# Kernel tuning notes

Measured on AMD Instinct MI355X. Metric: run time of the kernel, lower is better.

## Reference

```python
import jax, jax.numpy as jnp
import numpy as np

M0, M1, M2 = 128, 64, 32            # multiplicities of 0e, 1o, 2e
NUM_IRREPS = M0 + M1 + M2           # 224
NODE_DIM = 128
SPH_DIM = M0 + 3 * M1 + 5 * M2      # 480
HIDDEN = 2 * NODE_DIM + NUM_IRREPS  # 480
N = 100000
EPS = 1e-5
SQ3 = float(np.sqrt(3.0))
SQ5 = float(np.sqrt(5.0))


def _split(x):
    s0 = x[:, :M0]                                   # [N,128]   l=0
    s1 = x[:, M0:M0 + 3 * M1].reshape(-1, M1, 3)     # [N,64,3]  l=1
    s2 = x[:, M0 + 3 * M1:].reshape(-1, M2, 5)       # [N,32,5]  l=2
    return s0, s1, s2


def _merge(s0, s1, s2):
    n = s0.shape[0]
    return jnp.concatenate([s0, s1.reshape(n, -1), s2.reshape(n, -1)], axis=-1)


def _o3_linear(s0, s1, s2, w0, w1, w2, b0):
    # e3nn o3.Linear: one path per l, element path-normalization 1/sqrt(mul_in); bias only on 0e
    y0 = s0 @ w0 / np.float32(np.sqrt(M0)) + b0
    y1 = jnp.einsum('nik,io->nok', s1, w1) / np.float32(np.sqrt(M1))
    y2 = jnp.einsum('nik,io->nok', s2, w2) / np.float32(np.sqrt(M2))
    return y0, y1, y2


def _o3_layernorm(s0, s1, s2, w, b):
    # equivariant layer norm: mean-center scalars only; RMS over (mul, components) per irrep type
    f0 = s0 - jnp.mean(s0, axis=1, keepdims=True)
    n0 = jnp.mean(f0 * f0, axis=1, keepdims=True)
    f0 = f0 * jax.lax.rsqrt(n0 + EPS) * w[:M0] + b
    n1 = jnp.mean(s1 * s1, axis=(1, 2))[:, None, None]
    f1 = s1 * jax.lax.rsqrt(n1 + EPS) * w[M0:M0 + M1][None, :, None]
    n2 = jnp.mean(s2 * s2, axis=(1, 2))[:, None, None]
    f2 = s2 * jax.lax.rsqrt(n2 + EPS) * w[M0 + M1:][None, :, None]
    return f0, f1, f2


def setup_inputs() -> dict:
    key = jax.random.key(0)
    ks = jax.random.split(key, 16)
    g = lambda k, shape: jax.random.normal(k, shape, jnp.float32)
    return {
        'x_scalar': g(ks[0], (N, NODE_DIM)),
        'x_spherical': g(ks[1], (N, SPH_DIM)),
        'ln_g': jnp.ones((NODE_DIM,), jnp.float32),
        'ln_b': jnp.zeros((NODE_DIM,), jnp.float32),
        'o3n_w': jnp.ones((NUM_IRREPS,), jnp.float32),
        'o3n_b': jnp.zeros((M0,), jnp.float32),
        'U_w0': g(ks[2], (M0, M0)), 'U_w1': g(ks[3], (M1, M1)), 'U_w2': g(ks[4], (M2, M2)),
        'U_b0': jnp.zeros((M0,), jnp.float32),
        'V_w0': g(ks[5], (M0, M0)), 'V_w1': g(ks[6], (M1, M1)), 'V_w2': g(ks[7], (M2, M2)),
        'V_b0': jnp.zeros((M0,), jnp.float32),
        'dot_w': g(ks[8], (NUM_IRREPS, NODE_DIM)) / np.float32(np.sqrt(NUM_IRREPS)),
        'mlp_w1': g(ks[9], (NODE_DIM + NUM_IRREPS, NODE_DIM)) / np.float32(np.sqrt(NODE_DIM + NUM_IRREPS)),
        'mlp_b1': jnp.zeros((NODE_DIM,), jnp.float32),
        'mlp_w2': g(ks[10], (NODE_DIM, HIDDEN)) / np.float32(np.sqrt(NODE_DIM)),
        'mlp_b2': jnp.zeros((HIDDEN,), jnp.float32),
    }


def reference(x_scalar, x_spherical, ln_g, ln_b, o3n_w, o3n_b,
              U_w0, U_w1, U_w2, U_b0, V_w0, V_w1, V_w2, V_b0,
              dot_w, mlp_w1, mlp_b1, mlp_w2, mlp_b2):
    # scalar layer norm
    mu = jnp.mean(x_scalar, axis=-1, keepdims=True)
    var = jnp.var(x_scalar, axis=-1, keepdims=True)
    scalar_in = (x_scalar - mu) * jax.lax.rsqrt(var + EPS) * ln_g + ln_b
    # equivariant layer norm on spherical features
    s0, s1, s2 = _split(x_spherical)
    s0, s1, s2 = _o3_layernorm(s0, s1, s2, o3n_w, o3n_b)
    U0, U1, U2 = _o3_linear(s0, s1, s2, U_w0, U_w1, U_w2, U_b0)
    V0, V1, V2 = _o3_linear(s0, s1, s2, V_w0, V_w1, V_w2, V_b0)
    # o3.Norm: per-irrep L2 norm -> [N, 224]
    inv = jnp.concatenate([jnp.abs(V0),
                           jnp.sqrt(jnp.sum(V1 * V1, axis=-1)),
                           jnp.sqrt(jnp.sum(V2 * V2, axis=-1))], axis=-1)
    mlp_in = jnp.concatenate([scalar_in, inv], axis=-1)          # [N, 352]
    h = jax.nn.silu(mlp_in @ mlp_w1 + mlp_b1)
    mlp_out = h @ mlp_w2 + mlp_b2                                # [N, 480]
    a_vv = mlp_out[:, :NUM_IRREPS]
    a_sv = mlp_out[:, NUM_IRREPS:NUM_IRREPS + NODE_DIM]
    a_ss = mlp_out[:, NUM_IRREPS + NODE_DIM:]
    # ElementwiseTensorProduct with 224x0e: per-irrep scalar gating (net factor 1)
    d0 = U0 * a_vv[:, :M0]
    d1 = U1 * a_vv[:, M0:M0 + M1, None]
    d2 = U2 * a_vv[:, M0 + M1:, None]
    # EquivariantDot (component-normalized uuu TP to 0e): dot / sqrt(2l+1)
    dot = jnp.concatenate([U0 * V0,
                           jnp.sum(U1 * V1, axis=-1) / SQ3,
                           jnp.sum(U2 * V2, axis=-1) / SQ5], axis=-1)
    inner = dot @ dot_w                                           # [N, 128]
    d_scalar = a_sv * inner + a_ss
    return x_scalar + d_scalar, x_spherical + _merge(d0, d1, d2)
```

## Files before the change

kernel.cpp:

```cpp
#include <hip/hip_runtime.h>
#include <stdint.h>

typedef unsigned short u16;
typedef __attribute__((ext_vector_type(2))) unsigned short u16x2;
typedef __attribute__((ext_vector_type(4))) unsigned short u16x4;
typedef __attribute__((ext_vector_type(8))) short s16x8;
typedef __attribute__((ext_vector_type(2))) float f32x2;
typedef __attribute__((ext_vector_type(4))) float f32x4;

#define NROWS 100000
#define RPB   32
#define NBLK  (NROWS / RPB)
#define NTHR  512

#define PF   488
#define PS   360
#define PH   136
#define PD   232
#define PAB  484
#define PIF  132
#define FIN_RG  (16 * PF)
#define SCB_RG  (16 * PS)
#define HB_RG   (16 * PH)
#define DOT_RG  (16 * PD)
#define AOUT_RG (16 * PAB)
#define INN_RG  (16 * PIF)

#define OFF_FIN   0
#define OFF_AOUT  0
#define OFF_SCB   31232
#define OFF_INNER 31232
#define OFF_DOTB  54272
#define OFF_HB    69120
#define OFF_BCOM  77824
#define ARENA_SZ  79552

#define B_UW0 0
#define B_UW1 16384
#define B_UW2 20480
#define B_VW0 21504
#define B_VW1 37888
#define B_VW2 41984
#define B_DW  43008
#define B_W1  71680
#define B_W2  116736
#define PACK_TOT 178176

__device__ inline float bf2f(u16 u) {
    union { uint32_t i; float f; } v; v.i = (uint32_t)u << 16; return v.f;
}
__device__ inline u16 f2bf(float f) {
    union { float f; uint32_t i; } v; v.f = f;
    return (u16)((v.i + 0x7fffu + ((v.i >> 16) & 1u)) >> 16);
}
__device__ inline float wsum32(float v) {
    #pragma unroll
    for (int m = 16; m >= 1; m >>= 1) v += __shfl_xor(v, m);
    return v;
}
__device__ inline bool detect_f32(const void* xs) {
    const u16 v = ((const u16*)xs)[threadIdx.x & 63];
    const float f = bf2f(v);
    return __any(!(fabsf(f) < 1e10f)) != 0;
}
__device__ inline float ldin(const void* p, size_t i, bool f32) {
    return f32 ? ((const float*)p)[i] : bf2f(((const u16*)p)[i]);
}
__device__ inline void stout(void* p, size_t i, float v, bool f32) {
    if (f32) ((float*)p)[i] = v; else ((u16*)p)[i] = f2bf(v);
}

struct Ptrs {
    const void *xs, *xp, *lng, *lnb, *o3w, *o3b;
    const void *Uw0, *Uw1, *Uw2, *Ub0, *Vw0, *Vw1, *Vw2, *Vb0;
    const void *dw, *w1, *b1, *w2, *b2;
    const u16 *ws;
    void *out;
};

template<int KS, bool PACKED>
__device__ inline void load_b(const void* W, int D, int tile, int lane, bool wf32, s16x8* bfr)
{
    #pragma unroll
    for (int ks = 0; ks < KS; ++ks) {
        if (PACKED) {
            bfr[ks] = *(const s16x8*)((const u16*)W + (((size_t)tile * KS + ks) * 64 + (size_t)lane) * 8);
        } else {
            union { u16 u[8]; s16x8 v; } bb;
            const int k0 = ks * 32 + ((lane >> 4) << 3), o = tile * 16 + (lane & 15);
            #pragma unroll
            for (int j = 0; j < 8; ++j) {
                const size_t idx = (size_t)(k0 + j) * D + o;
                bb.u[j] = wf32 ? f2bf(((const float*)W)[idx]) : ((const u16*)W)[idx];
            }
            bfr[ks] = bb.v;
        }
    }
}

template<int KS>
__device__ inline f32x4 acc_ab(const u16* A, int pitchA, int lane, const s16x8* bfr)
{
    f32x4 acc = {0.f, 0.f, 0.f, 0.f};
    const u16* arow = A + (lane & 15) * pitchA + (lane >> 4) * 8;
    #pragma unroll
    for (int ks = 0; ks < KS; ++ks) {
        s16x8 a = *(const s16x8*)(arow + ks * 32);
        acc = __builtin_amdgcn_mfma_f32_16x16x32_bf16(a, bfr[ks], acc, 0, 0, 0);
    }
    return acc;
}

template<int KS, bool PACKED>
__device__ inline void mm_silu(const u16* A, int pitchA, const void* W, int D,
                               int tile, int lane, const u16* bias, u16* outH, bool wf32)
{
    s16x8 bfr[KS];
    load_b<KS, PACKED>(W, D, tile, lane, wf32, bfr);
    f32x4 acc = acc_ab<KS>(A, pitchA, lane, bfr);
    const int r = lane & 15, g = lane >> 4;
    const int o = tile * 16 + r;
    const float bv = bf2f(bias[o]);
    #pragma unroll
    for (int q = 0; q < 4; ++q) {
        float x = acc[q] + bv;
        outH[(g * 4 + q) * PH + o] = f2bf(x / (1.f + expf(-x)));
    }
}

__global__ void pack_weights(Ptrs P, u16* ws)
{
    const bool wf32 = detect_f32(P.xs);
    const int gid = blockIdx.x * 256 + threadIdx.x;
    if (gid >= PACK_TOT) return;
    const int  base[10] = {B_UW0, B_UW1, B_UW2, B_VW0, B_VW1, B_VW2, B_DW, B_W1, B_W2, PACK_TOT};
    const int  Kd[9]    = {128, 64, 32, 128, 64, 32, 224, 352, 128};
    const void* srcs[9] = {P.Uw0, P.Uw1, P.Uw2, P.Vw0, P.Vw1, P.Vw2, P.dw, P.w1, P.w2};
    const int  Dstride[9] = {128, 64, 32, 128, 64, 32, 128, 128, 480};
    int m = 0;
    for (int i = 1; i < 9; ++i) if (gid >= base[i]) m = i;
    const int e = gid - base[m];
    const int j = e & 7, lane = (e >> 3) & 63, tk = e >> 9;
    const int Ks = Kd[m] >> 5;
    const int ks = tk % Ks, tile = tk / Ks;
    const int k = ks * 32 + ((lane >> 4) << 3) + j;
    const int o = tile * 16 + (lane & 15);
    const size_t idx = (size_t)k * Dstride[m] + o;
    ws[gid] = wf32 ? f2bf(((const float*)srcs[m])[idx]) : ((const u16*)srcs[m])[idx];
}

template<int DT>
__device__ inline void stage1_core(const Ptrs& P, u16* fin0, u16* scb0, int tid, int row0)
{
    const int hw = tid >> 5, l32 = tid & 31;
    #pragma unroll
    for (int rg = 0; rg < 2; ++rg) {
        const int rr = hw + rg * 16;
        const size_t row = (size_t)(row0 + rr);
        u16* finr = fin0 + rg * FIN_RG + hw * PF;
        u16* scbr = scb0 + rg * SCB_RG + hw * PS;
        const u16*   xsb = (const u16*)P.xs + row * 128;
        const float* xsf = (const float*)P.xs + row * 128;
        const u16*   xpb = (const u16*)P.xp + row * 480;
        const float* xpf = (const float*)P.xp + row * 480;
        {
            float v[4];
            if (DT) { f32x4 u = *(const f32x4*)(xsf + l32 * 4); v[0]=u[0];v[1]=u[1];v[2]=u[2];v[3]=u[3]; }
            else    { u16x4 u = *(const u16x4*)(xsb + l32 * 4);
                      v[0]=bf2f(u[0]);v[1]=bf2f(u[1]);v[2]=bf2f(u[2]);v[3]=bf2f(u[3]); }
            float s  = v[0] + v[1] + v[2] + v[3];
            float s2 = v[0]*v[0] + v[1]*v[1] + v[2]*v[2] + v[3]*v[3];
            s = wsum32(s); s2 = wsum32(s2);
            const float mu = s * (1.f / 128.f);
            const float rs = 1.f / sqrtf(s2 * (1.f / 128.f) - mu * mu + 1e-5f);
            const int c = l32 * 4;
            #pragma unroll
            for (int j2 = 0; j2 < 4; ++j2)
                scbr[c + j2] =
                    f2bf((v[j2] - mu) * rs * ldin(P.lng, c + j2, DT) + ldin(P.lnb, c + j2, DT));
        }
        {
            float v[4];
            if (DT) { f32x4 u = *(const f32x4*)(xpf + l32 * 4); v[0]=u[0];v[1]=u[1];v[2]=u[2];v[3]=u[3]; }
            else    { u16x4 u = *(const u16x4*)(xpb + l32 * 4);
                      v[0]=bf2f(u[0]);v[1]=bf2f(u[1]);v[2]=bf2f(u[2]);v[3]=bf2f(u[3]); }
            float s  = v[0] + v[1] + v[2] + v[3];
            float s2 = v[0]*v[0] + v[1]*v[1] + v[2]*v[2] + v[3]*v[3];
            s = wsum32(s); s2 = wsum32(s2);
            const float mu = s * (1.f / 128.f);
            const float rs = 1.f / sqrtf(s2 * (1.f / 128.f) - mu * mu + 1e-5f);
            const int c = l32 * 4;
            #pragma unroll
            for (int j2 = 0; j2 < 4; ++j2)
                finr[c + j2] =
                    f2bf((v[j2] - mu) * rs * ldin(P.o3w, c + j2, DT) + ldin(P.o3b, c + j2, DT));
        }
        {
            const int cb = l32 * 6;
            float w[6];
            if (DT) {
                f32x2 a0 = *(const f32x2*)(xpf + 128 + cb);
                f32x2 a1 = *(const f32x2*)(xpf + 128 + cb + 2);
                f32x2 a2 = *(const f32x2*)(xpf + 128 + cb + 4);
                w[0]=a0[0]; w[1]=a0[1]; w[2]=a1[0]; w[3]=a1[1]; w[4]=a2[0]; w[5]=a2[1];
            } else {
                u16x2 a0 = *(const u16x2*)(xpb + 128 + cb);
                u16x2 a1 = *(const u16x2*)(xpb + 128 + cb + 2);
                u16x2 a2 = *(const u16x2*)(xpb + 128 + cb + 4);
                w[0]=bf2f(a0[0]); w[1]=bf2f(a0[1]); w[2]=bf2f(a1[0]);
                w[3]=bf2f(a1[1]); w[4]=bf2f(a2[0]); w[5]=bf2f(a2[1]);
            }
            float ss = 0.f;
            #pragma unroll
            for (int j2 = 0; j2 < 6; ++j2) ss += w[j2] * w[j2];
            ss = wsum32(ss);
            const float rs = 1.f / sqrtf(ss * (1.f / 192.f) + 1e-5f);
            #pragma unroll
            for (int j2 = 0; j2 < 6; ++j2) {
                const int c = cb + j2, i = c / 3, k = c - 3 * i;
                finr[128 + k * 64 + i] = f2bf(w[j2] * rs * ldin(P.o3w, 128 + i, DT));
            }
        }
        {
            const int cb = l32 * 5;
            float w[5];
            #pragma unroll
            for (int j2 = 0; j2 < 5; ++j2)
                w[j2] = DT ? xpf[320 + cb + j2] : bf2f(xpb[320 + cb + j2]);
            float ss = 0.f;
            #pragma unroll
            for (int j2 = 0; j2 < 5; ++j2) ss += w[j2] * w[j2];
            ss = wsum32(ss);
            const float rs = 1.f / sqrtf(ss * (1.f / 160.f) + 1e-5f);
            #pragma unroll
            for (int j2 = 0; j2 < 5; ++j2) {
                const int c = cb + j2, i = c / 5, k = c - 5 * i;
                finr[320 + k * 32 + i] = f2bf(w[j2] * rs * ldin(P.o3w, 192 + i, DT));
            }
        }
    }
}

template<bool PACKED>
__global__ __launch_bounds__(NTHR, 4) void xpainn_main(Ptrs P)
{
    __shared__ __align__(16) unsigned char arena[ARENA_SZ];
    u16*   fin    = (u16*)(arena + OFF_FIN);
    u16*   aoutB  = (u16*)(arena + OFF_AOUT);
    u16*   scb    = (u16*)(arena + OFF_SCB);
    float* innerF = (float*)(arena + OFF_INNER);
    u16*   dotb   = (u16*)(arena + OFF_DOTB);
    u16*   hb     = (u16*)(arena + OFF_HB);
    u16*   bcom   = (u16*)(arena + OFF_BCOM);

    const int tid = threadIdx.x;
    const int lane = tid & 63, wave = tid >> 6;
    const int r = lane & 15, g = lane >> 4;
    const int row0 = blockIdx.x * RPB;
    const bool isf32 = detect_f32(P.xs);

    for (int i = tid; i < 864; i += NTHR) {
        const void* src; int off;
        if (i < 128)      { src = P.Ub0; off = i; }
        else if (i < 256) { src = P.Vb0; off = i - 128; }
        else if (i < 384) { src = P.b1;  off = i - 256; }
        else              { src = P.b2;  off = i - 384; }
        bcom[i] = f2bf(ldin(src, off, isf32));
    }
    if (isf32) stage1_core<1>(P, fin, scb, tid, row0);
    else       stage1_core<0>(P, fin, scb, tid, row0);
    __syncthreads();

    float u0r[2][4];
    float uxr[2][5][4];
    {
        s16x8 bU[4], bV[4];
        load_b<4, PACKED>(PACKED ? (const void*)(P.ws + B_UW0) : P.Uw0, 128, wave, lane, isf32, bU);
        load_b<4, PACKED>(PACKED ? (const void*)(P.ws + B_VW0) : P.Vw0, 128, wave, lane, isf32, bV);
        const int o = wave * 16 + r;
        const float bu = bf2f(bcom[o]), bv = bf2f(bcom[128 + o]);
        #pragma unroll
        for (int rg = 0; rg < 2; ++rg) {
            f32x4 au = acc_ab<4>(fin + rg * FIN_RG, PF, lane, bU);
            f32x4 av = acc_ab<4>(fin + rg * FIN_RG, PF, lane, bV);
            u16* scbR = scb + rg * SCB_RG;
            u16* dotR = dotb + rg * DOT_RG;
            #pragma unroll
            for (int q = 0; q < 4; ++q) {
                const float U = au[q] * 0.08838834764831845f + bu;
                const float V = av[q] * 0.08838834764831845f + bv;
                u0r[rg][q] = U;
                const int lrow = g * 4 + q;
                scbR[lrow * PS + 128 + o] = f2bf(fabsf(V));
                dotR[lrow * PD + o]       = f2bf(U * V);
            }
        }
    }
    if (wave < 4) {
        const int tt = wave, o = tt * 16 + r;
        float sv[2][4] = {{0.f,0.f,0.f,0.f},{0.f,0.f,0.f,0.f}};
        float suv[2][4] = {{0.f,0.f,0.f,0.f},{0.f,0.f,0.f,0.f}};
        #pragma unroll
        for (int ch = 0; ch < 3; ++ch) {
            s16x8 bU[2], bV[2];
            load_b<2, PACKED>(PACKED ? (const void*)(P.ws + B_UW1) : P.Uw1, 64, tt, lane, isf32, bU);
            load_b<2, PACKED>(PACKED ? (const void*)(P.ws + B_VW1) : P.Vw1, 64, tt, lane, isf32, bV);
            #pragma unroll
            for (int rg = 0; rg < 2; ++rg) {
                f32x4 au = acc_ab<2>(fin + rg * FIN_RG + 128 + 64 * ch, PF, lane, bU);
                f32x4 av = acc_ab<2>(fin + rg * FIN_RG + 128 + 64 * ch, PF, lane, bV);
                #pragma unroll
                for (int q = 0; q < 4; ++q) {
                    const float U = au[q] * 0.125f, V = av[q] * 0.125f;
                    uxr[rg][ch][q] = U; sv[rg][q] += V * V; suv[rg][q] += U * V;
                }
            }
        }
        #pragma unroll
        for (int rg = 0; rg < 2; ++rg) {
            #pragma unroll
            for (int q = 0; q < 4; ++q) {
                const int lrow = g * 4 + q;
                (scb + rg * SCB_RG)[lrow * PS + 256 + o]  = f2bf(sqrtf(sv[rg][q]));
                (dotb + rg * DOT_RG)[lrow * PD + 128 + o] = f2bf(suv[rg][q] * 0.5773502691896258f);
            }
        }
    } else if (wave < 6) {
        const int tt = wave - 4, o = tt * 16 + r;
        float sv[2][4] = {{0.f,0.f,0.f,0.f},{0.f,0.f,0.f,0.f}};
        float suv[2][4] = {{0.f,0.f,0.f,0.f},{0.f,0.f,0.f,0.f}};
        #pragma unroll
        for (int ch = 0; ch < 5; ++ch) {
            s16x8 bU[1], bV[1];
            load_b<1, PACKED>(PACKED ? (const void*)(P.ws + B_UW2) : P.Uw2, 32, tt, lane, isf32, bU);
            load_b<1, PACKED>(PACKED ? (const void*)(P.ws + B_VW2) : P.Vw2, 32, tt, lane, isf32, bV);
            #pragma unroll
            for (int rg = 0; rg < 2; ++rg) {
                f32x4 au = acc_ab<1>(fin + rg * FIN_RG + 320 + 32 * ch, PF, lane, bU);
                f32x4 av = acc_ab<1>(fin + rg * FIN_RG + 320 + 32 * ch, PF, lane, bV);
                #pragma unroll
                for (int q = 0; q < 4; ++q) {
                    const float U = au[q] * 0.17677669529663687f, V = av[q] * 0.17677669529663687f;
                    uxr[rg][ch][q] = U; sv[rg][q] += V * V; suv[rg][q] += U * V;
                }
            }
        }
        #pragma unroll
        for (int rg = 0; rg < 2; ++rg) {
            #pragma unroll
            for (int q = 0; q < 4; ++q) {
                const int lrow = g * 4 + q;
                (scb + rg * SCB_RG)[lrow * PS + 320 + o]  = f2bf(sqrtf(sv[rg][q]));
                (dotb + rg * DOT_RG)[lrow * PD + 192 + o] = f2bf(suv[rg][q] * 0.4472135954999579f);
            }
        }
    }
    __syncthreads();

    #pragma unroll
    for (int rg = 0; rg < 2; ++rg)
        mm_silu<11, PACKED>(scb + rg * SCB_RG, PS, PACKED ? (const void*)(P.ws + B_W1) : P.w1,
                            128, wave, lane, bcom + 256, hb + rg * HB_RG, isf32);
    __syncthreads();

    for (int ti = wave; ti < 38; ti += 8) {
        if (ti < 30) {
            s16x8 bfr[4];
            load_b<4, PACKED>(PACKED ? (const void*)(P.ws + B_W2) : P.w2, 480, ti, lane, isf32, bfr);
            const int o = ti * 16 + r;
            const float bv = bf2f(bcom[384 + o]);
            #pragma unroll
            for (int rg = 0; rg < 2; ++rg) {
                f32x4 acc = acc_ab<4>(hb + rg * HB_RG, PH, lane, bfr);
                u16* aoutR = aoutB + rg * AOUT_RG;
                #pragma unroll
                for (int q = 0; q < 4; ++q)
                    aoutR[(g * 4 + q) * PAB + o] = f2bf(acc[q] + bv);
            }
        } else {
            s16x8 bfr[7];
            load_b<7, PACKED>(PACKED ? (const void*)(P.ws + B_DW) : P.dw, 128, ti - 30, lane, isf32, bfr);
            const int o = (ti - 30) * 16 + r;
            #pragma unroll
            for (int rg = 0; rg < 2; ++rg) {
                f32x4 acc = acc_ab<7>(dotb + rg * DOT_RG, PD, lane, bfr);
                float* innR = innerF + rg * INN_RG;
                #pragma unroll
                for (int q = 0; q < 4; ++q)
                    innR[(g * 4 + q) * PIF + o] = acc[q];
            }
        }
    }
    __syncthreads();

    #pragma unroll
    for (int it = 0; it < 2; ++it) {
        const int idx = tid + it * NTHR;
        const int r2 = idx >> 5, c4 = (idx & 31) * 4;
        const u16*  aoutR = aoutB + (r2 >> 4) * AOUT_RG + (r2 & 15) * PAB;
        const float* innR = innerF + (r2 >> 4) * INN_RG + (r2 & 15) * PIF;
        const size_t gb = (size_t)(row0 + r2) * 128 + c4;
        const u16x4 asv = *(const u16x4*)(aoutR + 224 + c4);
        const u16x4 ass = *(const u16x4*)(aoutR + 352 + c4);
        const f32x4 inn = *(const f32x4*)(innR + c4);
        if (isf32) {
            const f32x4 xs = *(const f32x4*)((const float*)P.xs + gb);
            f32x4 o;
            #pragma unroll
            for (int j = 0; j < 4; ++j) o[j] = xs[j] + bf2f(asv[j]) * inn[j] + bf2f(ass[j]);
            *(f32x4*)((float*)P.out + gb) = o;
        } else {
            const u16x4 xs = *(const u16x4*)((const u16*)P.xs + gb);
            u16x4 o;
            #pragma unroll
            for (int j = 0; j < 4; ++j) o[j] = f2bf(bf2f(xs[j]) + bf2f(asv[j]) * inn[j] + bf2f(ass[j]));
            *(u16x4*)((u16*)P.out + gb) = o;
        }
    }
    {
        const size_t ob = (size_t)NROWS * 128;
        #pragma unroll
        for (int rg = 0; rg < 2; ++rg) {
            const u16* aoutR = aoutB + rg * AOUT_RG;
            const int o = wave * 16 + r;
            #pragma unroll
            for (int q = 0; q < 4; ++q) {
                const int lrow = g * 4 + q;
                const size_t gr = (size_t)(row0 + rg * 16 + lrow) * 480;
                const float av = bf2f(aoutR[lrow * PAB + o]);
                stout(P.out, ob + gr + o, ldin(P.xp, gr + o, isf32) + u0r[rg][q] * av, isf32);
            }
            if (wave < 4) {
                const int i = wave * 16 + r;
                #pragma unroll
                for (int q = 0; q < 4; ++q) {
                    const int lrow = g * 4 + q;
                    const size_t gr = (size_t)(row0 + rg * 16 + lrow) * 480;
                    const float av = bf2f(aoutR[lrow * PAB + 128 + i]);
                    #pragma unroll
                    for (int ch = 0; ch < 3; ++ch) {
                        const size_t c = 128 + 3 * i + ch;
                        stout(P.out, ob + gr + c, ldin(P.xp, gr + c, isf32) + uxr[rg][ch][q] * av, isf32);
                    }
                }
            } else if (wave < 6) {
                const int i = (wave - 4) * 16 + r;
                #pragma unroll
                for (int q = 0; q < 4; ++q) {
                    const int lrow = g * 4 + q;
                    const size_t gr = (size_t)(row0 + rg * 16 + lrow) * 480;
                    const float av = bf2f(aoutR[lrow * PAB + 192 + i]);
                    #pragma unroll
                    for (int ch = 0; ch < 5; ++ch) {
                        const size_t c = 320 + 5 * i + ch;
                        stout(P.out, ob + gr + c, ldin(P.xp, gr + c, isf32) + uxr[rg][ch][q] * av, isf32);
                    }
                }
            }
        }
    }
}

extern "C" void kernel_launch(void* const* d_in, const int* in_sizes, int n_in,
                              void* d_out, int out_size, void* d_ws, size_t ws_size,
                              hipStream_t stream)
{
    Ptrs P;
    P.xs  = d_in[0];  P.xp  = d_in[1];
    P.lng = d_in[2];  P.lnb = d_in[3];
    P.o3w = d_in[4];  P.o3b = d_in[5];
    P.Uw0 = d_in[6];  P.Uw1 = d_in[7];
    P.Uw2 = d_in[8];  P.Ub0 = d_in[9];
    P.Vw0 = d_in[10]; P.Vw1 = d_in[11];
    P.Vw2 = d_in[12]; P.Vb0 = d_in[13];
    P.dw  = d_in[14]; P.w1  = d_in[15];
    P.b1  = d_in[16]; P.w2  = d_in[17];
    P.b2  = d_in[18];
    P.ws  = (const u16*)d_ws;
    P.out = d_out;

    const bool packed = (ws_size >= (size_t)PACK_TOT * sizeof(u16));
    if (packed) {
        pack_weights<<<(PACK_TOT + 255) / 256, 256, 0, stream>>>(P, (u16*)d_ws);
        xpainn_main<true><<<NBLK, NTHR, 0, stream>>>(P);
    } else {
        xpainn_main<false><<<NBLK, NTHR, 0, stream>>>(P);
    }
}
```

Before: 235.9 us.

## Specialize for fp32 I/O, use hardware bf16 converts, fuse spherical output into MLP stage

Drops runtime bf16/fp32 detection and assumes fp32 inputs and outputs, removing per-element dtype branches. Replaces the software bf16 rounding with the v_cvt_pk_bf16_f32 instruction and packs pairs of bf16 stores, and vectorizes the l=1/l=2 loads. Restructures the second MLP matmul so each wave keeps its a_vv gate tiles in registers and writes the spherical output right away, skipping the bf16 round trip through LDS for those gates. This loses the bf16 input path and changes gate precision slightly.

Measured after the change: 220.3 us, median of 2. 6.6% less time.

```diff
diff --git a/kernel.cpp b/kernel.cpp
--- a/kernel.cpp
+++ b/kernel.cpp
@@ -2,11 +2,11 @@
 #include <stdint.h>
 
 typedef unsigned short u16;
-typedef __attribute__((ext_vector_type(2))) unsigned short u16x2;
 typedef __attribute__((ext_vector_type(4))) unsigned short u16x4;
 typedef __attribute__((ext_vector_type(8))) short s16x8;
 typedef __attribute__((ext_vector_type(2))) float f32x2;
 typedef __attribute__((ext_vector_type(4))) float f32x4;
+typedef __attribute__((ext_vector_type(4), aligned(4))) float f32x4u;
 
 #define NROWS 100000
 #define RPB   32
@@ -50,36 +50,27 @@
     union { uint32_t i; float f; } v; v.i = (uint32_t)u << 16; return v.f;
 }
 __device__ inline u16 f2bf(float f) {
-    union { float f; uint32_t i; } v; v.f = f;
-    return (u16)((v.i + 0x7fffu + ((v.i >> 16) & 1u)) >> 16);
+    uint32_t d; asm("v_cvt_pk_bf16_f32 %0, %1, %1" : "=v"(d) : "v"(f)); return (u16)d;
+}
+__device__ inline uint32_t cvtpk(float lo, float hi) {
+    uint32_t d; asm("v_cvt_pk_bf16_f32 %0, %1, %2" : "=v"(d) : "v"(lo), "v"(hi)); return d;
 }
 __device__ inline float wsum32(float v) {
     #pragma unroll
     for (int m = 16; m >= 1; m >>= 1) v += __shfl_xor(v, m);
     return v;
 }
-__device__ inline bool detect_f32(const void* xs) {
-    const u16 v = ((const u16*)xs)[threadIdx.x & 63];
-    const float f = bf2f(v);
-    return __any(!(fabsf(f) < 1e10f)) != 0;
-}
-__device__ inline float ldin(const void* p, size_t i, bool f32) {
-    return f32 ? ((const float*)p)[i] : bf2f(((const u16*)p)[i]);
-}
-__device__ inline void stout(void* p, size_t i, float v, bool f32) {
-    if (f32) ((float*)p)[i] = v; else ((u16*)p)[i] = f2bf(v);
-}
 
 struct Ptrs {
-    const void *xs, *xp, *lng, *lnb, *o3w, *o3b;
-    const void *Uw0, *Uw1, *Uw2, *Ub0, *Vw0, *Vw1, *Vw2, *Vb0;
-    const void *dw, *w1, *b1, *w2, *b2;
+    const float *xs, *xp, *lng, *lnb, *o3w, *o3b;
+    const float *Uw0, *Uw1, *Uw2, *Ub0, *Vw0, *Vw1, *Vw2, *Vb0;
+    const float *dw, *w1, *b1, *w2, *b2;
     const u16 *ws;
-    void *out;
+    float *out;
 };
 
 template<int KS, bool PACKED>
-__device__ inline void load_b(const void* W, int D, int tile, int lane, bool wf32, s16x8* bfr)
+__device__ inline void load_b(const void* W, int D, int tile, int lane, s16x8* bfr)
 {
     #pragma unroll
     for (int ks = 0; ks < KS; ++ks) {
@@ -89,10 +80,8 @@
             union { u16 u[8]; s16x8 v; } bb;
             const int k0 = ks * 32 + ((lane >> 4) << 3), o = tile * 16 + (lane & 15);
             #pragma unroll
-            for (int j = 0; j < 8; ++j) {
-                const size_t idx = (size_t)(k0 + j) * D + o;
-                bb.u[j] = wf32 ? f2bf(((const float*)W)[idx]) : ((const u16*)W)[idx];
-            }
+            for (int j = 0; j < 8; ++j)
+                bb.u[j] = f2bf(((const float*)W)[(size_t)(k0 + j) * D + o]);
             bfr[ks] = bb.v;
         }
     }
@@ -111,31 +100,13 @@
     return acc;
 }
 
-template<int KS, bool PACKED>
-__device__ inline void mm_silu(const u16* A, int pitchA, const void* W, int D,
-                               int tile, int lane, const u16* bias, u16* outH, bool wf32)
-{
-    s16x8 bfr[KS];
-    load_b<KS, PACKED>(W, D, tile, lane, wf32, bfr);
-    f32x4 acc = acc_ab<KS>(A, pitchA, lane, bfr);
-    const int r = lane & 15, g = lane >> 4;
-    const int o = tile * 16 + r;
-    const float bv = bf2f(bias[o]);
-    #pragma unroll
-    for (int q = 0; q < 4; ++q) {
-        float x = acc[q] + bv;
-        outH[(g * 4 + q) * PH + o] = f2bf(x / (1.f + expf(-x)));
-    }
-}
-
 __global__ void pack_weights(Ptrs P, u16* ws)
 {
-    const bool wf32 = detect_f32(P.xs);
     const int gid = blockIdx.x * 256 + threadIdx.x;
     if (gid >= PACK_TOT) return;
     const int  base[10] = {B_UW0, B_UW1, B_UW2, B_VW0, B_VW1, B_VW2, B_DW, B_W1, B_W2, PACK_TOT};
     const int  Kd[9]    = {128, 64, 32, 128, 64, 32, 224, 352, 128};
-    const void* srcs[9] = {P.Uw0, P.Uw1, P.Uw2, P.Vw0, P.Vw1, P.Vw2, P.dw, P.w1, P.w2};
+    const float* srcs[9] = {P.Uw0, P.Uw1, P.Uw2, P.Vw0, P.Vw1, P.Vw2, P.dw, P.w1, P.w2};
     const int  Dstride[9] = {128, 64, 32, 128, 64, 32, 128, 128, 480};
     int m = 0;
     for (int i = 1; i < 9; ++i) if (gid >= base[i]) m = i;
@@ -145,11 +116,9 @@
     const int ks = tk % Ks, tile = tk / Ks;
     const int k = ks * 32 + ((lane >> 4) << 3) + j;
     const int o = tile * 16 + (lane & 15);
-    const size_t idx = (size_t)k * Dstride[m] + o;
-    ws[gid] = wf32 ? f2bf(((const float*)srcs[m])[idx]) : ((const u16*)srcs[m])[idx];
-}
-
-template<int DT>
+    ws[gid] = f2bf(srcs[m][(size_t)k * Dstride[m] + o]);
+}
+
 __device__ inline void stage1_core(const Ptrs& P, u16* fin0, u16* scb0, int tid, int row0)
 {
     const int hw = tid >> 5, l32 = tid & 31;
@@ -159,57 +128,43 @@
         const size_t row = (size_t)(row0 + rr);
         u16* finr = fin0 + rg * FIN_RG + hw * PF;
         u16* scbr = scb0 + rg * SCB_RG + hw * PS;
-        const u16*   xsb = (const u16*)P.xs + row * 128;
-        const float* xsf = (const float*)P.xs + row * 128;
-        const u16*   xpb = (const u16*)P.xp + row * 480;
-        const float* xpf = (const float*)P.xp + row * 480;
-        {
-            float v[4];
-            if (DT) { f32x4 u = *(const f32x4*)(xsf + l32 * 4); v[0]=u[0];v[1]=u[1];v[2]=u[2];v[3]=u[3]; }
-            else    { u16x4 u = *(const u16x4*)(xsb + l32 * 4);
-                      v[0]=bf2f(u[0]);v[1]=bf2f(u[1]);v[2]=bf2f(u[2]);v[3]=bf2f(u[3]); }
-            float s  = v[0] + v[1] + v[2] + v[3];
-            float s2 = v[0]*v[0] + v[1]*v[1] + v[2]*v[2] + v[3]*v[3];
+        const float* xsf = P.xs + row * 128;
+        const float* xpf = P.xp + row * 480;
+        {
+            f32x4 u = *(const f32x4*)(xsf + l32 * 4);
+            float s  = u[0] + u[1] + u[2] + u[3];
+            float s2 = u[0]*u[0] + u[1]*u[1] + u[2]*u[2] + u[3]*u[3];
             s = wsum32(s); s2 = wsum32(s2);
             const float mu = s * (1.f / 128.f);
             const float rs = 1.f / sqrtf(s2 * (1.f / 128.f) - mu * mu + 1e-5f);
             const int c = l32 * 4;
+            float t[4];
             #pragma unroll
             for (int j2 = 0; j2 < 4; ++j2)
-                scbr[c + j2] =
-                    f2bf((v[j2] - mu) * rs * ldin(P.lng, c + j2, DT) + ldin(P.lnb, c + j2, DT));
-        }
-        {
-            float v[4];
-            if (DT) { f32x4 u = *(const f32x4*)(xpf + l32 * 4); v[0]=u[0];v[1]=u[1];v[2]=u[2];v[3]=u[3]; }
-            else    { u16x4 u = *(const u16x4*)(xpb + l32 * 4);
-                      v[0]=bf2f(u[0]);v[1]=bf2f(u[1]);v[2]=bf2f(u[2]);v[3]=bf2f(u[3]); }
-            float s  = v[0] + v[1] + v[2] + v[3];
-            float s2 = v[0]*v[0] + v[1]*v[1] + v[2]*v[2] + v[3]*v[3];
+                t[j2] = (u[j2] - mu) * rs * P.lng[c + j2] + P.lnb[c + j2];
+            *(uint32_t*)(scbr + c)     = cvtpk(t[0], t[1]);
+            *(uint32_t*)(scbr + c + 2) = cvtpk(t[2], t[3]);
+        }
+        {
+            f32x4 u = *(const f32x4*)(xpf + l32 * 4);
+            float s  = u[0] + u[1] + u[2] + u[3];
+            float s2 = u[0]*u[0] + u[1]*u[1] + u[2]*u[2] + u[3]*u[3];
             s = wsum32(s); s2 = wsum32(s2);
             const float mu = s * (1.f / 128.f);
             const float rs = 1.f / sqrtf(s2 * (1.f / 128.f) - mu * mu + 1e-5f);
             const int c = l32 * 4;
+            float t[4];
             #pragma unroll
             for (int j2 = 0; j2 < 4; ++j2)
-                finr[c + j2] =
-                    f2bf((v[j2] - mu) * rs * ldin(P.o3w, c + j2, DT) + ldin(P.o3b, c + j2, DT));
+                t[j2] = (u[j2] - mu) * rs * P.o3w[c + j2] + P.o3b[c + j2];
+            *(uint32_t*)(finr + c)     = cvtpk(t[0], t[1]);
+            *(uint32_t*)(finr + c + 2) = cvtpk(t[2], t[3]);
         }
         {
             const int cb = l32 * 6;
-            float w[6];
-            if (DT) {
-                f32x2 a0 = *(const f32x2*)(xpf + 128 + cb);
-                f32x2 a1 = *(const f32x2*)(xpf + 128 + cb + 2);
-                f32x2 a2 = *(const f32x2*)(xpf + 128 + cb + 4);
-                w[0]=a0[0]; w[1]=a0[1]; w[2]=a1[0]; w[3]=a1[1]; w[4]=a2[0]; w[5]=a2[1];
-            } else {
-                u16x2 a0 = *(const u16x2*)(xpb + 128 + cb);
-                u16x2 a1 = *(const u16x2*)(xpb + 128 + cb + 2);
-                u16x2 a2 = *(const u16x2*)(xpb + 128 + cb + 4);
-                w[0]=bf2f(a0[0]); w[1]=bf2f(a0[1]); w[2]=bf2f(a1[0]);
-                w[3]=bf2f(a1[1]); w[4]=bf2f(a2[0]); w[5]=bf2f(a2[1]);
-            }
+            f32x4u a = *(const f32x4u*)(xpf + 128 + cb);
+            f32x2  b = *(const f32x2*)(xpf + 128 + cb + 4);
+            float w[6] = {a[0], a[1], a[2], a[3], b[0], b[1]};
             float ss = 0.f;
             #pragma unroll
             for (int j2 = 0; j2 < 6; ++j2) ss += w[j2] * w[j2];
@@ -218,15 +173,13 @@
             #pragma unroll
             for (int j2 = 0; j2 < 6; ++j2) {
                 const int c = cb + j2, i = c / 3, k = c - 3 * i;
-                finr[128 + k * 64 + i] = f2bf(w[j2] * rs * ldin(P.o3w, 128 + i, DT));
+                finr[128 + k * 64 + i] = f2bf(w[j2] * rs * P.o3w[128 + i]);
             }
         }
         {
             const int cb = l32 * 5;
-            float w[5];
-            #pragma unroll
-            for (int j2 = 0; j2 < 5; ++j2)
-                w[j2] = DT ? xpf[320 + cb + j2] : bf2f(xpb[320 + cb + j2]);
+            f32x4u a = *(const f32x4u*)(xpf + 320 + cb);
+            float w[5] = {a[0], a[1], a[2], a[3], xpf[320 + cb + 4]};
             float ss = 0.f;
             #pragma unroll
             for (int j2 = 0; j2 < 5; ++j2) ss += w[j2] * w[j2];
@@ -235,7 +188,7 @@
             #pragma unroll
             for (int j2 = 0; j2 < 5; ++j2) {
                 const int c = cb + j2, i = c / 5, k = c - 5 * i;
-                finr[320 + k * 32 + i] = f2bf(w[j2] * rs * ldin(P.o3w, 192 + i, DT));
+                finr[320 + k * 32 + i] = f2bf(w[j2] * rs * P.o3w[192 + i]);
             }
         }
     }
@@ -257,26 +210,24 @@
     const int lane = tid & 63, wave = tid >> 6;
     const int r = lane & 15, g = lane >> 4;
     const int row0 = blockIdx.x * RPB;
-    const bool isf32 = detect_f32(P.xs);
 
     for (int i = tid; i < 864; i += NTHR) {
-        const void* src; int off;
+        const float* src; int off;
         if (i < 128)      { src = P.Ub0; off = i; }
         else if (i < 256) { src = P.Vb0; off = i - 128; }
         else if (i < 384) { src = P.b1;  off = i - 256; }
         else              { src = P.b2;  off = i - 384; }
-        bcom[i] = f2bf(ldin(src, off, isf32));
-    }
-    if (isf32) stage1_core<1>(P, fin, scb, tid, row0);
-    else       stage1_core<0>(P, fin, scb, tid, row0);
+        bcom[i] = f2bf(src[off]);
+    }
+    stage1_core(P, fin, scb, tid, row0);
     __syncthreads();
 
     float u0r[2][4];
     float uxr[2][5][4];
     {
         s16x8 bU[4], bV[4];
-        load_b<4, PACKED>(PACKED ? (const void*)(P.ws + B_UW0) : P.Uw0, 128, wave, lane, isf32, bU);
-        load_b<4, PACKED>(PACKED ? (const void*)(P.ws + B_VW0) : P.Vw0, 128, wave, lane, isf32, bV);
+        load_b<4, PACKED>(PACKED ? (const void*)(P.ws + B_UW0) : (const void*)P.Uw0, 128, wave, lane, bU);
+        load_b<4, PACKED>(PACKED ? (const void*)(P.ws + B_VW0) : (const void*)P.Vw0, 128, wave, lane, bV);
         const int o = wave * 16 + r;
         const float bu = bf2f(bcom[o]), bv = bf2f(bcom[128 + o]);
         #pragma unroll
@@ -303,8 +254,8 @@
         #pragma unroll
         for (int ch = 0; ch < 3; ++ch) {
             s16x8 bU[2], bV[2];
-            load_b<2, PACKED>(PACKED ? (const void*)(P.ws + B_UW1) : P.Uw1, 64, tt, lane, isf32, bU);
-            load_b<2, PACKED>(PACKED ? (const void*)(P.ws + B_VW1) : P.Vw1, 64, tt, lane, isf32, bV);
+            load_b<2, PACKED>(PACKED ? (const void*)(P.ws + B_UW1) : (const void*)P.Uw1, 64, tt, lane, bU);
+            load_b<2, PACKED>(PACKED ? (const void*)(P.ws + B_VW1) : (const void*)P.Vw1, 64, tt, lane, bV);
             #pragma unroll
             for (int rg = 0; rg < 2; ++rg) {
                 f32x4 au = acc_ab<2>(fin + rg * FIN_RG + 128 + 64 * ch, PF, lane, bU);
@@ -332,8 +283,8 @@
         #pragma unroll
         for (int ch = 0; ch < 5; ++ch) {
             s16x8 bU[1], bV[1];
-            load_b<1, PACKED>(PACKED ? (const void*)(P.ws + B_UW2) : P.Uw2, 32, tt, lane, isf32, bU);
-            load_b<1, PACKED>(PACKED ? (const void*)(P.ws + B_VW2) : P.Vw2, 32, tt, lane, isf32, bV);
+            load_b<1, PACKED>(PACKED ? (const void*)(P.ws + B_UW2) : (const void*)P.Uw2, 32, tt, lane, bU);
+            load_b<1, PACKED>(PACKED ? (const void*)(P.ws + B_VW2) : (const void*)P.Vw2, 32, tt, lane, bV);
             #pragma unroll
             for (int rg = 0; rg < 2; ++rg) {
                 f32x4 au = acc_ab<1>(fin + rg * FIN_RG + 320 + 32 * ch, PF, lane, bU);
@@ -358,36 +309,115 @@
     __syncthreads();
 
     #pragma unroll
-    for (int rg = 0; rg < 2; ++rg)
-        mm_silu<11, PACKED>(scb + rg * SCB_RG, PS, PACKED ? (const void*)(P.ws + B_W1) : P.w1,
-                            128, wave, lane, bcom + 256, hb + rg * HB_RG, isf32);
+    for (int rg = 0; rg < 2; ++rg) {
+        s16x8 bfr[11];
+        load_b<11, PACKED>(PACKED ? (const void*)(P.ws + B_W1) : (const void*)P.w1, 128, wave, lane, bfr);
+        f32x4 acc = acc_ab<11>(scb + rg * SCB_RG, PS, lane, bfr);
+        const int o = wave * 16 + r;
+        const float bv = bf2f(bcom[256 + o]);
+        #pragma unroll
+        for (int q = 0; q < 4; ++q) {
+            float x = acc[q] + bv;
+            hb[rg * HB_RG + (g * 4 + q) * PH + o] = f2bf(x / (1.f + expf(-x)));
+        }
+    }
     __syncthreads();
 
-    for (int ti = wave; ti < 38; ti += 8) {
-        if (ti < 30) {
+    {
+        float avv0[2][4], avv1[2][4];
+        {
             s16x8 bfr[4];
-            load_b<4, PACKED>(PACKED ? (const void*)(P.ws + B_W2) : P.w2, 480, ti, lane, isf32, bfr);
+            load_b<4, PACKED>(PACKED ? (const void*)(P.ws + B_W2) : (const void*)P.w2, 480, wave, lane, bfr);
+            const int o = wave * 16 + r;
+            const float bv = bf2f(bcom[384 + o]);
+            #pragma unroll
+            for (int rg = 0; rg < 2; ++rg) {
+                f32x4 acc = acc_ab<4>(hb + rg * HB_RG, PH, lane, bfr);
+                #pragma unroll
+                for (int q = 0; q < 4; ++q) avv0[rg][q] = acc[q] + bv;
+            }
+        }
+        {
+            const int ti = wave + 8;
+            s16x8 bfr[4];
+            load_b<4, PACKED>(PACKED ? (const void*)(P.ws + B_W2) : (const void*)P.w2, 480, ti, lane, bfr);
             const int o = ti * 16 + r;
             const float bv = bf2f(bcom[384 + o]);
             #pragma unroll
             for (int rg = 0; rg < 2; ++rg) {
                 f32x4 acc = acc_ab<4>(hb + rg * HB_RG, PH, lane, bfr);
-                u16* aoutR = aoutB + rg * AOUT_RG;
-                #pragma unroll
-                for (int q = 0; q < 4; ++q)
-                    aoutR[(g * 4 + q) * PAB + o] = f2bf(acc[q] + bv);
-            }
-        } else {
-            s16x8 bfr[7];
-            load_b<7, PACKED>(PACKED ? (const void*)(P.ws + B_DW) : P.dw, 128, ti - 30, lane, isf32, bfr);
-            const int o = (ti - 30) * 16 + r;
+                if (wave < 6) {
+                    #pragma unroll
+                    for (int q = 0; q < 4; ++q) avv1[rg][q] = acc[q] + bv;
+                } else {
+                    u16* aoutR = aoutB + rg * AOUT_RG;
+                    #pragma unroll
+                    for (int q = 0; q < 4; ++q)
+                        aoutR[(g * 4 + q) * PAB + o] = f2bf(acc[q] + bv);
+                }
+            }
+        }
+        {
+            const size_t ob = (size_t)NROWS * 128;
             #pragma unroll
             for (int rg = 0; rg < 2; ++rg) {
-                f32x4 acc = acc_ab<7>(dotb + rg * DOT_RG, PD, lane, bfr);
-                float* innR = innerF + rg * INN_RG;
-                #pragma unroll
-                for (int q = 0; q < 4; ++q)
-                    innR[(g * 4 + q) * PIF + o] = acc[q];
+                const int o = wave * 16 + r;
+                #pragma unroll
+                for (int q = 0; q < 4; ++q) {
+                    const size_t gr = (size_t)(row0 + rg * 16 + g * 4 + q) * 480;
+                    P.out[ob + gr + o] = P.xp[gr + o] + u0r[rg][q] * avv0[rg][q];
+                }
+                if (wave < 4) {
+                    const int i = wave * 16 + r;
+                    #pragma unroll
+                    for (int q = 0; q < 4; ++q) {
+                        const size_t gr = (size_t)(row0 + rg * 16 + g * 4 + q) * 480;
+                        #pragma unroll
+                        for (int ch = 0; ch < 3; ++ch) {
+                            const size_t c = 128 + 3 * i + ch;
+                            P.out[ob + gr + c] = P.xp[gr + c] + uxr[rg][ch][q] * avv1[rg][q];
+                        }
+                    }
+                } else if (wave < 6) {
+                    const int i = (wave - 4) * 16 + r;
+                    #pragma unroll
+                    for (int q = 0; q < 4; ++q) {
+                        const size_t gr = (size_t)(row0 + rg * 16 + g * 4 + q) * 480;
+                        #pragma unroll
+                        for (int ch = 0; ch < 5; ++ch) {
+                            const size_t c = 320 + 5 * i + ch;
+                            P.out[ob + gr + c] = P.xp[gr + c] + uxr[rg][ch][q] * avv1[rg][q];
+                        }
+                    }
+                }
+            }
+        }
+        for (int ti = wave + 16; ti < 38; ti += 8) {
+            if (ti < 30) {
+                s16x8 bfr[4];
+                load_b<4, PACKED>(PACKED ? (const void*)(P.ws + B_W2) : (const void*)P.w2, 480, ti, lane, bfr);
+                const int o = ti * 16 + r;
+                const float bv = bf2f(bcom[384 + o]);
+                #pragma unroll
+                for (int rg = 0; rg < 2; ++rg) {
+                    f32x4 acc = acc_ab<4>(hb + rg * HB_RG, PH, lane, bfr);
+                    u16* aoutR = aoutB + rg * AOUT_RG;
+                    #pragma unroll
+                    for (int q = 0; q < 4; ++q)
+                        aoutR[(g * 4 + q) * PAB + o] = f2bf(acc[q] + bv);
+                }
+            } else {
+                s16x8 bfr[7];
+                load_b<7, PACKED>(PACKED ? (const void*)(P.ws + B_DW) : (const void*)P.dw, 128, ti - 30, lane, bfr);
+                const int oo = (ti - 30) * 16 + r;
+                #pragma unroll
+                for (int rg = 0; rg < 2; ++rg) {
+                    f32x4 acc = acc_ab<7>(dotb + rg * DOT_RG, PD, lane, bfr);
+                    float* innR = innerF + rg * INN_RG;
+                    #pragma unroll
+                    for (int q = 0; q < 4; ++q)
+                        innR[(g * 4 + q) * PIF + oo] = acc[q];
+                }
             }
         }
     }
@@ -403,61 +433,11 @@
         const u16x4 asv = *(const u16x4*)(aoutR + 224 + c4);
         const u16x4 ass = *(const u16x4*)(aoutR + 352 + c4);
         const f32x4 inn = *(const f32x4*)(innR + c4);
-        if (isf32) {
-            const f32x4 xs = *(const f32x4*)((const float*)P.xs + gb);
-            f32x4 o;
-            #pragma unroll
-            for (int j = 0; j < 4; ++j) o[j] = xs[j] + bf2f(asv[j]) * inn[j] + bf2f(ass[j]);
-            *(f32x4*)((float*)P.out + gb) = o;
-        } else {
-            const u16x4 xs = *(const u16x4*)((const u16*)P.xs + gb);
-            u16x4 o;
-            #pragma unroll
-            for (int j = 0; j < 4; ++j) o[j] = f2bf(bf2f(xs[j]) + bf2f(asv[j]) * inn[j] + bf2f(ass[j]));
-            *(u16x4*)((u16*)P.out + gb) = o;
-        }
-    }
-    {
-        const size_t ob = (size_t)NROWS * 128;
-        #pragma unroll
-        for (int rg = 0; rg < 2; ++rg) {
-            const u16* aoutR = aoutB + rg * AOUT_RG;
-            const int o = wave * 16 + r;
-            #pragma unroll
-            for (int q = 0; q < 4; ++q) {
-                const int lrow = g * 4 + q;
-                const size_t gr = (size_t)(row0 + rg * 16 + lrow) * 480;
-                const float av = bf2f(aoutR[lrow * PAB + o]);
-                stout(P.out, ob + gr + o, ldin(P.xp, gr + o, isf32) + u0r[rg][q] * av, isf32);
-            }
-            if (wave < 4) {
-                const int i = wave * 16 + r;
-                #pragma unroll
-                for (int q = 0; q < 4; ++q) {
-                    const int lrow = g * 4 + q;
-                    const size_t gr = (size_t)(row0 + rg * 16 + lrow) * 480;
-                    const float av = bf2f(aoutR[lrow * PAB + 128 + i]);
-                    #pragma unroll
-                    for (int ch = 0; ch < 3; ++ch) {
-                        const size_t c = 128 + 3 * i + ch;
-                        stout(P.out, ob + gr + c, ldin(P.xp, gr + c, isf32) + uxr[rg][ch][q] * av, isf32);
-                    }
-                }
-            } else if (wave < 6) {
-                const int i = (wave - 4) * 16 + r;
-                #pragma unroll
-                for (int q = 0; q < 4; ++q) {
-                    const int lrow = g * 4 + q;
-                    const size_t gr = (size_t)(row0 + rg * 16 + lrow) * 480;
-                    const float av = bf2f(aoutR[lrow * PAB + 192 + i]);
-                    #pragma unroll
-                    for (int ch = 0; ch < 5; ++ch) {
-                        const size_t c = 320 + 5 * i + ch;
-                        stout(P.out, ob + gr + c, ldin(P.xp, gr + c, isf32) + uxr[rg][ch][q] * av, isf32);
-                    }
-                }
-            }
-        }
+        const f32x4 xs = *(const f32x4*)(P.xs + gb);
+        f32x4 o;
+        #pragma unroll
+        for (int j = 0; j < 4; ++j) o[j] = xs[j] + bf2f(asv[j]) * inn[j] + bf2f(ass[j]);
+        *(f32x4*)(P.out + gb) = o;
     }
 }
 
@@ -466,18 +446,18 @@
                               hipStream_t stream)
 {
     Ptrs P;
-    P.xs  = d_in[0];  P.xp  = d_in[1];
-    P.lng = d_in[2];  P.lnb = d_in[3];
-    P.o3w = d_in[4];  P.o3b = d_in[5];
-    P.Uw0 = d_in[6];  P.Uw1 = d_in[7];
-    P.Uw2 = d_in[8];  P.Ub0 = d_in[9];
-    P.Vw0 = d_in[10]; P.Vw1 = d_in[11];
-    P.Vw2 = d_in[12]; P.Vb0 = d_in[13];
-    P.dw  = d_in[14]; P.w1  = d_in[15];
-    P.b1  = d_in[16]; P.w2  = d_in[17];
-    P.b2  = d_in[18];
+    P.xs  = (const float*)d_in[0];  P.xp  = (const float*)d_in[1];
+    P.lng = (const float*)d_in[2];  P.lnb = (const float*)d_in[3];
+    P.o3w = (const float*)d_in[4];  P.o3b = (const float*)d_in[5];
+    P.Uw0 = (const float*)d_in[6];  P.Uw1 = (const float*)d_in[7];
+    P.Uw2 = (const float*)d_in[8];  P.Ub0 = (const float*)d_in[9];
+    P.Vw0 = (const float*)d_in[10]; P.Vw1 = (const float*)d_in[11];
+    P.Vw2 = (const float*)d_in[12]; P.Vb0 = (const float*)d_in[13];
+    P.dw  = (const float*)d_in[14]; P.w1  = (const float*)d_in[15];
+    P.b1  = (const float*)d_in[16]; P.w2  = (const float*)d_in[17];
+    P.b2  = (const float*)d_in[18];
     P.ws  = (const u16*)d_ws;
-    P.out = d_out;
+    P.out = (float*)d_out;
 
     const bool packed = (ws_size >= (size_t)PACK_TOT * sizeof(u16));
     if (packed) {
```
